# Kernel tuning notes

Hardware: AMD Instinct MI355X
Metric: run time of the kernel (lower is better)

## Reference

```python
import jax, jax.numpy as jnp
import numpy as np

N, M, D = 8192, 8192, 256

def setup_inputs() -> dict:
    key = jax.random.key(0)
    k1, k2, k3, k4 = jax.random.split(key, 4)
    x1 = jax.random.normal(k1, (N, D), dtype=jnp.float32)
    x2 = jax.random.normal(k2, (M, D), dtype=jnp.float32)
    alpha_raw = jax.random.normal(k3, (D,), dtype=jnp.float32)      # nn.Parameter(torch.randn(input_dim))
    variance_raw = jnp.ones((1,), dtype=jnp.float32)                # nn.Parameter(torch.ones(1))
    return {"x1": x1, "x2": x2, "alpha_raw": alpha_raw, "variance_raw": variance_raw}

def reference(x1, x2, alpha_raw, variance_raw):
    # alpha = softmax(alpha_raw^2), variance = variance_raw^2
    alpha = jax.nn.softmax(alpha_raw ** 2)                          # (D,)
    variance = variance_raw ** 2                                    # (1,)
    # GEMM rewrite of sum_d alpha_d (x1_i - x2_j)^2:
    #   ||x1*sqrt(a)||^2 - 2 (x1*sqrt(a))(x2*sqrt(a))^T + ||x2*sqrt(a)||^2
    sa = jnp.sqrt(alpha)
    a = x1 * sa                                                     # (N, D)
    b = x2 * sa                                                     # (M, D)
    sq = (jnp.sum(a * a, axis=-1)[:, None]
          - 2.0 * (a @ b.T)
          + jnp.sum(b * b, axis=-1)[None, :])                       # (N, M)
    sq = jnp.maximum(sq, 0.0)  # numerical guard; exact value is non-negative
    kernel = variance * jnp.exp(-0.5 * sq)                          # (N, M)
    if kernel.shape[0] == 1:
        kernel = jnp.squeeze(kernel)
    return kernel
```

## Files before the change

kernel.cpp:

```cpp
#include <hip/hip_runtime.h>
#include <stdint.h>

#define NROWS 8192
#define MCOLS 8192
#define KDIM  256

typedef __bf16 bf16x8 __attribute__((ext_vector_type(8)));
typedef float  floatx4 __attribute__((ext_vector_type(4)));

__device__ __forceinline__ unsigned short f32_to_bf16_rne(float f) {
    unsigned int u = __float_as_uint(f);
    u += 0x7FFFu + ((u >> 16) & 1u);
    return (unsigned short)(u >> 16);
}
__device__ __forceinline__ float bf16_to_f32(unsigned short h) {
    return __uint_as_float(((unsigned int)h) << 16);
}

__device__ __forceinline__ void async16(const void* g, void* l) {
    __builtin_amdgcn_global_load_lds(
        (const __attribute__((address_space(1))) unsigned int*)g,
        (__attribute__((address_space(3))) unsigned int*)l,
        16, 0, 0);
}

__global__ void prep_alpha(const float* __restrict__ araw, float* __restrict__ sa) {
    __shared__ float buf[256];
    int d = threadIdx.x;
    float z = araw[d];
    z = z * z;
    buf[d] = z;
    __syncthreads();
    for (int s = 128; s > 0; s >>= 1) {
        if (d < s) buf[d] = fmaxf(buf[d], buf[d + s]);
        __syncthreads();
    }
    float mx = buf[0];
    __syncthreads();
    float e = __expf(z - mx);
    buf[d] = e;
    __syncthreads();
    for (int s = 128; s > 0; s >>= 1) {
        if (d < s) buf[d] += buf[d + s];
        __syncthreads();
    }
    float sum = buf[0];
    sa[d] = sqrtf(e / sum);
}

__global__ void prep_rows(const float* __restrict__ x, const float* __restrict__ sa,
                          unsigned short* __restrict__ mat, float* __restrict__ rnorm) {
    __shared__ float buf[256];
    int row = blockIdx.x;
    int d = threadIdx.x;
    float v = x[(size_t)row * KDIM + d] * sa[d];
    unsigned short h = f32_to_bf16_rne(v);
    mat[(size_t)row * KDIM + d] = h;
    float fv = bf16_to_f32(h);
    buf[d] = fv * fv;
    __syncthreads();
    for (int s = 128; s > 0; s >>= 1) {
        if (d < s) buf[d] += buf[d + s];
        __syncthreads();
    }
    if (d == 0) rnorm[row] = buf[0];
}

__global__ __launch_bounds__(256) void rbf_gemm(
    const unsigned short* __restrict__ A, const unsigned short* __restrict__ B,
    const float* __restrict__ ra, const float* __restrict__ rb,
    const float* __restrict__ vraw, float* __restrict__ out)
{
    __shared__ unsigned short As[128 * 64];
    __shared__ unsigned short Bs[128 * 64];

    const int tid  = threadIdx.x;
    const int lane = tid & 63;
    const int wave = tid >> 6;
    const int bm = blockIdx.y;
    const int bn = blockIdx.x;
    const int wm = (wave & 1) * 64;
    const int wn = (wave >> 1) * 64;
    const int quad = lane >> 4;
    const int l15  = lane & 15;

    floatx4 acc[4][4];
#pragma unroll
    for (int i = 0; i < 4; i++)
#pragma unroll
        for (int j = 0; j < 4; j++) acc[i][j] = (floatx4)0.0f;

    for (int k0 = 0; k0 < KDIM; k0 += 64) {
#pragma unroll
        for (int it = 0; it < 4; ++it) {
            int c   = it * 256 + tid;
            int row = c >> 3;
            int kc  = c & 7;
            int gkc = kc ^ (row & 7);
            const unsigned short* gA = A + (size_t)(bm * 128 + row) * KDIM + k0 + gkc * 8;
            const unsigned short* gB = B + (size_t)(bn * 128 + row) * KDIM + k0 + gkc * 8;
            async16(gA, &As[c * 8]);
            async16(gB, &Bs[c * 8]);
        }
        __syncthreads();

#pragma unroll
        for (int ks = 0; ks < 2; ++ks) {
            bf16x8 af[4], bfr[4];
            int kc = ks * 4 + quad;
#pragma unroll
            for (int t = 0; t < 4; ++t) {
                int m  = wm + t * 16 + l15;
                int sa_ = m * 8 + (kc ^ (m & 7));
                af[t]  = *(const bf16x8*)&As[sa_ * 8];
                int n  = wn + t * 16 + l15;
                int sb_ = n * 8 + (kc ^ (n & 7));
                bfr[t] = *(const bf16x8*)&Bs[sb_ * 8];
            }
#pragma unroll
            for (int ti = 0; ti < 4; ++ti)
#pragma unroll
                for (int tj = 0; tj < 4; ++tj)
                    acc[ti][tj] = __builtin_amdgcn_mfma_f32_16x16x32_bf16(
                        af[ti], bfr[tj], acc[ti][tj], 0, 0, 0);
        }
        __syncthreads();
    }

    float variance = vraw[0] * vraw[0];
    float rbv[4];
#pragma unroll
    for (int tj = 0; tj < 4; ++tj) rbv[tj] = rb[bn * 128 + wn + tj * 16 + l15];
#pragma unroll
    for (int ti = 0; ti < 4; ++ti) {
        int rowbase = bm * 128 + wm + ti * 16 + quad * 4;
        float rav[4];
#pragma unroll
        for (int r = 0; r < 4; ++r) rav[r] = ra[rowbase + r];
#pragma unroll
        for (int tj = 0; tj < 4; ++tj) {
            int col = bn * 128 + wn + tj * 16 + l15;
#pragma unroll
            for (int r = 0; r < 4; ++r) {
                float s = rav[r] + rbv[tj] - 2.0f * acc[ti][tj][r];
                s = fmaxf(s, 0.0f);
                out[(size_t)(rowbase + r) * MCOLS + col] = variance * __expf(-0.5f * s);
            }
        }
    }
}

extern "C" void kernel_launch(void* const* d_in, const int* in_sizes, int n_in,
                              void* d_out, int out_size, void* d_ws, size_t ws_size,
                              hipStream_t stream) {
    const float* x1   = (const float*)d_in[0];
    const float* x2   = (const float*)d_in[1];
    const float* araw = (const float*)d_in[2];
    const float* vraw = (const float*)d_in[3];
    float* out = (float*)d_out;

    char* ws = (char*)d_ws;
    float* sa = (float*)ws;
    float* ra = (float*)(ws + 1024);
    float* rb = (float*)(ws + 1024 + 32768);
    unsigned short* Amat = (unsigned short*)(ws + 66560);
    unsigned short* Bmat = (unsigned short*)(ws + 66560 + (size_t)NROWS * KDIM * 2);

    prep_alpha<<<1, 256, 0, stream>>>(araw, sa);
    prep_rows<<<NROWS, 256, 0, stream>>>(x1, sa, Amat, ra);
    prep_rows<<<MCOLS, 256, 0, stream>>>(x2, sa, Bmat, rb);

    dim3 grid(MCOLS / 128, NROWS / 128);
    rbf_gemm<<<grid, 256, 0, stream>>>(Amat, Bmat, ra, rb, vraw, out);
}
```

Before: 307.7 us.

## Double-buffer GEMM tiles, remap blocks per XCD, nontemporal stores, merge prep kernels

```diff
diff --git a/kernel.cpp b/kernel.cpp
--- a/kernel.cpp
+++ b/kernel.cpp
@@ -25,45 +25,47 @@
 }
 
 __global__ void prep_alpha(const float* __restrict__ araw, float* __restrict__ sa) {
-    __shared__ float buf[256];
     int d = threadIdx.x;
     float z = araw[d];
     z = z * z;
-    buf[d] = z;
+    float m = z;
+#pragma unroll
+    for (int off = 32; off; off >>= 1) m = fmaxf(m, __shfl_xor(m, off));
+    __shared__ float wred[4];
+    if ((d & 63) == 0) wred[d >> 6] = m;
     __syncthreads();
-    for (int s = 128; s > 0; s >>= 1) {
-        if (d < s) buf[d] = fmaxf(buf[d], buf[d + s]);
-        __syncthreads();
-    }
-    float mx = buf[0];
+    float mx = fmaxf(fmaxf(wred[0], wred[1]), fmaxf(wred[2], wred[3]));
+    float e = __expf(z - mx);
+    float s = e;
+#pragma unroll
+    for (int off = 32; off; off >>= 1) s += __shfl_xor(s, off);
     __syncthreads();
-    float e = __expf(z - mx);
-    buf[d] = e;
+    if ((d & 63) == 0) wred[d >> 6] = s;
     __syncthreads();
-    for (int s = 128; s > 0; s >>= 1) {
-        if (d < s) buf[d] += buf[d + s];
-        __syncthreads();
-    }
-    float sum = buf[0];
+    float sum = wred[0] + wred[1] + wred[2] + wred[3];
     sa[d] = sqrtf(e / sum);
 }
 
-__global__ void prep_rows(const float* __restrict__ x, const float* __restrict__ sa,
-                          unsigned short* __restrict__ mat, float* __restrict__ rnorm) {
-    __shared__ float buf[256];
-    int row = blockIdx.x;
+__global__ void prep_rows(const float* __restrict__ x1, const float* __restrict__ x2,
+                          const float* __restrict__ sa,
+                          unsigned short* __restrict__ Amat, unsigned short* __restrict__ Bmat,
+                          float* __restrict__ ra, float* __restrict__ rb) {
+    int blk = blockIdx.x;
+    const float* x; unsigned short* mat; float* nrm; int row;
+    if (blk < NROWS) { x = x1; mat = Amat; nrm = ra; row = blk; }
+    else             { x = x2; mat = Bmat; nrm = rb; row = blk - NROWS; }
     int d = threadIdx.x;
     float v = x[(size_t)row * KDIM + d] * sa[d];
     unsigned short h = f32_to_bf16_rne(v);
     mat[(size_t)row * KDIM + d] = h;
     float fv = bf16_to_f32(h);
-    buf[d] = fv * fv;
+    float p = fv * fv;
+#pragma unroll
+    for (int off = 32; off; off >>= 1) p += __shfl_xor(p, off);
+    __shared__ float wred[4];
+    if ((d & 63) == 0) wred[d >> 6] = p;
     __syncthreads();
-    for (int s = 128; s > 0; s >>= 1) {
-        if (d < s) buf[d] += buf[d + s];
-        __syncthreads();
-    }
-    if (d == 0) rnorm[row] = buf[0];
+    if (d == 0) nrm[row] = wred[0] + wred[1] + wred[2] + wred[3];
 }
 
 __global__ __launch_bounds__(256) void rbf_gemm(
@@ -71,14 +73,19 @@
     const float* __restrict__ ra, const float* __restrict__ rb,
     const float* __restrict__ vraw, float* __restrict__ out)
 {
-    __shared__ unsigned short As[128 * 64];
-    __shared__ unsigned short Bs[128 * 64];
+    __shared__ unsigned short As[2][128 * 64];
+    __shared__ unsigned short Bs[2][128 * 64];
 
     const int tid  = threadIdx.x;
     const int lane = tid & 63;
     const int wave = tid >> 6;
-    const int bm = blockIdx.y;
-    const int bn = blockIdx.x;
+
+    const int g   = blockIdx.y * gridDim.x + blockIdx.x;
+    const int xcd = g & 7;
+    const int i   = g >> 3;
+    const int bm  = (xcd >> 2) * 32 + (i >> 4);
+    const int bn  = (xcd & 3) * 16 + (i & 15);
+
     const int wm = (wave & 1) * 64;
     const int wn = (wave >> 1) * 64;
     const int quad = lane >> 4;
@@ -86,11 +93,11 @@
 
     floatx4 acc[4][4];
 #pragma unroll
-    for (int i = 0; i < 4; i++)
+    for (int ti = 0; ti < 4; ti++)
 #pragma unroll
-        for (int j = 0; j < 4; j++) acc[i][j] = (floatx4)0.0f;
+        for (int tj = 0; tj < 4; tj++) acc[ti][tj] = (floatx4)0.0f;
 
-    for (int k0 = 0; k0 < KDIM; k0 += 64) {
+    auto stage = [&](int buf, int k0) {
 #pragma unroll
         for (int it = 0; it < 4; ++it) {
             int c   = it * 256 + tid;
@@ -99,23 +106,31 @@
             int gkc = kc ^ (row & 7);
             const unsigned short* gA = A + (size_t)(bm * 128 + row) * KDIM + k0 + gkc * 8;
             const unsigned short* gB = B + (size_t)(bn * 128 + row) * KDIM + k0 + gkc * 8;
-            async16(gA, &As[c * 8]);
-            async16(gB, &Bs[c * 8]);
+            async16(gA, &As[buf][c * 8]);
+            async16(gB, &Bs[buf][c * 8]);
         }
-        __syncthreads();
+    };
 
+    stage(0, 0);
+    __syncthreads();
+
+#pragma unroll
+    for (int t = 0; t < 4; ++t) {
+        if (t < 3) stage((t + 1) & 1, (t + 1) * 64);
+        const unsigned short* Ab = As[t & 1];
+        const unsigned short* Bb = Bs[t & 1];
 #pragma unroll
         for (int ks = 0; ks < 2; ++ks) {
             bf16x8 af[4], bfr[4];
             int kc = ks * 4 + quad;
 #pragma unroll
-            for (int t = 0; t < 4; ++t) {
-                int m  = wm + t * 16 + l15;
-                int sa_ = m * 8 + (kc ^ (m & 7));
-                af[t]  = *(const bf16x8*)&As[sa_ * 8];
-                int n  = wn + t * 16 + l15;
-                int sb_ = n * 8 + (kc ^ (n & 7));
-                bfr[t] = *(const bf16x8*)&Bs[sb_ * 8];
+            for (int tt = 0; tt < 4; ++tt) {
+                int m   = wm + tt * 16 + l15;
+                int sA  = m * 8 + (kc ^ (m & 7));
+                af[tt]  = *(const bf16x8*)&Ab[sA * 8];
+                int n   = wn + tt * 16 + l15;
+                int sB  = n * 8 + (kc ^ (n & 7));
+                bfr[tt] = *(const bf16x8*)&Bb[sB * 8];
             }
 #pragma unroll
             for (int ti = 0; ti < 4; ++ti)
@@ -124,7 +139,7 @@
                     acc[ti][tj] = __builtin_amdgcn_mfma_f32_16x16x32_bf16(
                         af[ti], bfr[tj], acc[ti][tj], 0, 0, 0);
         }
-        __syncthreads();
+        if (t < 3) __syncthreads();
     }
 
     float variance = vraw[0] * vraw[0];
@@ -144,7 +159,8 @@
             for (int r = 0; r < 4; ++r) {
                 float s = rav[r] + rbv[tj] - 2.0f * acc[ti][tj][r];
                 s = fmaxf(s, 0.0f);
-                out[(size_t)(rowbase + r) * MCOLS + col] = variance * __expf(-0.5f * s);
+                float val = variance * __expf(-0.5f * s);
+                __builtin_nontemporal_store(val, &out[(size_t)(rowbase + r) * MCOLS + col]);
             }
         }
     }
@@ -167,8 +183,7 @@
     unsigned short* Bmat = (unsigned short*)(ws + 66560 + (size_t)NROWS * KDIM * 2);
 
     prep_alpha<<<1, 256, 0, stream>>>(araw, sa);
-    prep_rows<<<NROWS, 256, 0, stream>>>(x1, sa, Amat, ra);
-    prep_rows<<<MCOLS, 256, 0, stream>>>(x2, sa, Bmat, rb);
+    prep_rows<<<NROWS + MCOLS, 256, 0, stream>>>(x1, x2, sa, Amat, Bmat, ra, rb);
 
     dim3 grid(MCOLS / 128, NROWS / 128);
     rbf_gemm<<<grid, 256, 0, stream>>>(Amat, Bmat, ra, rb, vraw, out);
```

Result: slower. 316.0 us (+2.7%).
